# Kernel tuning notes

Measured on AMD Instinct MI355X. Metric: run time of the kernel, lower is better.

The kernel has to match this reference:

```python
import jax, jax.numpy as jnp
import numpy as np

B = 8192
D = 1024        # input_size
HID = 1024      # hidden_size
H = 8           # num_heads
HS = HID // H   # head_size = 128
P = int(HID * (4.0 / 3.0))  # 1365
K = 4           # causal conv kernel size


def _linear_params(key, fan_in, shape_w, shape_b):
    kw, kb = jax.random.split(key)
    s = 1.0 / np.sqrt(fan_in)
    w = jax.random.uniform(kw, shape_w, jnp.float32, -s, s)
    b = jax.random.uniform(kb, shape_b, jnp.float32, -s, s)
    return w, b


def setup_inputs() -> dict:
    key = jax.random.key(0)
    ks = jax.random.split(key, 20)
    inp = {
        'x': jax.random.normal(ks[0], (B, D), jnp.float32),
        'h_prev': jax.random.normal(ks[1], (B, HID), jnp.float32),
        'c_prev': jnp.zeros((B, HID), jnp.float32),
        'n_prev': jnp.ones((B, HID), jnp.float32),
        'm_prev': jnp.zeros((B, HID), jnp.float32),
        'rms_w': jnp.ones((D,), jnp.float32),
    }
    # causal conv: Conv1d(1,1,4) -> weight [4], bias scalar
    cw, cb = _linear_params(ks[2], K, (K,), ())
    inp['conv_w'], inp['conv_b'] = cw, cb
    # block-diagonal input projections: [H, D/H, HID/H] stored as x @ W (already transposed)
    names_in = ['Wz', 'Wi', 'Wf', 'Wo']
    for i, nm in enumerate(names_in):
        w, b = _linear_params(ks[3 + i], D // H, (H, D // H, HS), (HID,))
        inp[nm + '_w'], inp[nm + '_b'] = w, b
    names_rec = ['Rz', 'Ri', 'Rf', 'Ro']
    for i, nm in enumerate(names_rec):
        w, b = _linear_params(ks[7 + i], HS, (H, HS, HS), (HID,))
        inp[nm + '_w'], inp[nm + '_b'] = w, b
    inp['gn_w'] = jnp.ones((HID,), jnp.float32)
    inp['gn_b'] = jnp.zeros((HID,), jnp.float32)
    w, b = _linear_params(ks[11], HID, (HID, P), (P,))
    inp['upL_w'], inp['upL_b'] = w, b
    w, b = _linear_params(ks[12], HID, (HID, P), (P,))
    inp['upR_w'], inp['upR_b'] = w, b
    w, b = _linear_params(ks[13], P, (P, D), (D,))
    inp['down_w'], inp['down_b'] = w, b
    return inp


def _block_diag(x, w, b, num_blocks):
    # x: [B, F_in]; w: [H, F_in/H, F_out/H]; b: [F_out]
    bsz = x.shape[0]
    xh = x.reshape(bsz, num_blocks, -1)
    y = jnp.einsum('bhd,hde->bhe', xh, w)
    return y.reshape(bsz, -1) + b


def _rmsnorm(x, w, eps=1e-6):
    return x * jax.lax.rsqrt(jnp.mean(x * x, axis=-1, keepdims=True) + eps) * w


def _groupnorm(x, w, b, num_groups, eps=1e-5):
    bsz, C = x.shape
    xg = x.reshape(bsz, num_groups, -1)
    mu = jnp.mean(xg, axis=-1, keepdims=True)
    var = jnp.mean(jnp.square(xg - mu), axis=-1, keepdims=True)
    xn = (xg - mu) * jax.lax.rsqrt(var + eps)
    return xn.reshape(bsz, C) * w + b


def _causal_conv(x, w, b):
    # x: [B, L]; cross-correlation with left pad K-1 (matches Conv1d pad=3 then [:-3])
    L = x.shape[1]
    xp = jnp.pad(x, ((0, 0), (K - 1, 0)))
    out = b
    for k in range(K):
        out = out + w[k] * xp[:, k:k + L]
    return out


def reference(x, h_prev, c_prev, n_prev, m_prev, rms_w, conv_w, conv_b,
              Wz_w, Wz_b, Wi_w, Wi_b, Wf_w, Wf_b, Wo_w, Wo_b,
              Rz_w, Rz_b, Ri_w, Ri_b, Rf_w, Rf_b, Ro_w, Ro_b,
              gn_w, gn_b, upL_w, upL_b, upR_w, upR_b, down_w, down_b):
    x_norm = _rmsnorm(x, rms_w)
    x_conv = jax.nn.silu(_causal_conv(x_norm, conv_w, conv_b))

    z = jnp.tanh(_block_diag(x, Wz_w, Wz_b, H) + _block_diag(h_prev, Rz_w, Rz_b, H))
    o = jax.nn.sigmoid(_block_diag(x, Wo_w, Wo_b, H) + _block_diag(h_prev, Ro_w, Ro_b, H))
    i_tilde = _block_diag(x_conv, Wi_w, Wi_b, H) + _block_diag(h_prev, Ri_w, Ri_b, H)
    f_tilde = _block_diag(x_conv, Wf_w, Wf_b, H) + _block_diag(h_prev, Rf_w, Rf_b, H)

    m_t = jnp.maximum(f_tilde + m_prev, i_tilde)
    i_g = jnp.exp(i_tilde - m_t)
    f_g = jnp.exp(f_tilde + m_prev - m_t)
    c_t = f_g * c_prev + i_g * z
    n_t = f_g * n_prev + i_g
    h_t = o * c_t / n_t

    out_norm = _groupnorm(h_t, gn_w, gn_b, H)
    left = out_norm @ upL_w + upL_b
    right = out_norm @ upR_w + upR_b
    out = (left * jax.nn.gelu(right, approximate=False)) @ down_w + down_b
    final_output = out + x
    return (final_output, h_t, c_t, n_t, m_t)
```

## Files before the change

### kernel.cpp

```cpp
#include <hip/hip_runtime.h>
#include <hip/hip_bf16.h>
#include <math.h>

typedef __attribute__((ext_vector_type(8))) short bf16x8;
typedef __attribute__((ext_vector_type(4))) float f32x4;

#define BSZ   8192
#define DIM   1024
#define HIDN  1024
#define NH    8
#define HSZ   128
#define PN    1365
#define PPAD  1408

#define MFMA16(a, b, c) __builtin_amdgcn_mfma_f32_16x16x32_bf16(a, b, c, 0, 0, 0)

__device__ __forceinline__ void gload_lds16(const void* g, void* l) {
    __builtin_amdgcn_global_load_lds(
        (const __attribute__((address_space(1))) unsigned int*)(unsigned long long)g,
        (__attribute__((address_space(3))) unsigned int*)(unsigned int)(unsigned long long)l,
        16, 0, 0);
}

__device__ __forceinline__ void split_bf16(float v, __hip_bfloat16* hi, __hip_bfloat16* lo) {
    __hip_bfloat16 h = __float2bfloat16(v);
    *hi = h;
    *lo = __float2bfloat16(v - __bfloat162float(h));
}

__global__ __launch_bounds__(256) void k_rms_conv(
    const float* __restrict__ x, const float* __restrict__ rms_w,
    const float* __restrict__ conv_w, const float* __restrict__ conv_b,
    float* __restrict__ x_conv)
{
    __shared__ float xn[3 + DIM];
    __shared__ float red[4];
    const int row = blockIdx.x;
    const int t = threadIdx.x;
    const float* xr = x + (size_t)row * DIM;

    float4 v = *(const float4*)(xr + t * 4);
    float ss = v.x * v.x + v.y * v.y + v.z * v.z + v.w * v.w;
    #pragma unroll
    for (int off = 32; off; off >>= 1) ss += __shfl_down(ss, off);
    if ((t & 63) == 0) red[t >> 6] = ss;
    if (t < 3) xn[t] = 0.0f;
    __syncthreads();
    float tot = red[0] + red[1] + red[2] + red[3];
    float scale = rsqrtf(tot * (1.0f / (float)DIM) + 1e-6f);

    float4 w = *(const float4*)(rms_w + t * 4);
    xn[3 + t * 4 + 0] = v.x * scale * w.x;
    xn[3 + t * 4 + 1] = v.y * scale * w.y;
    xn[3 + t * 4 + 2] = v.z * scale * w.z;
    xn[3 + t * 4 + 3] = v.w * scale * w.w;
    __syncthreads();

    const float cw0 = conv_w[0], cw1 = conv_w[1], cw2 = conv_w[2], cw3 = conv_w[3];
    const float cb = conv_b[0];
    float4 o;
    float* op = (float*)&o;
    #pragma unroll
    for (int j = 0; j < 4; ++j) {
        int l = t * 4 + j;
        float val = cb + cw0 * xn[l] + cw1 * xn[l + 1] + cw2 * xn[l + 2] + cw3 * xn[l + 3];
        op[j] = val * (1.0f / (1.0f + expf(-val)));
    }
    *(float4*)(x_conv + (size_t)row * DIM + t * 4) = o;
}

#define TB2 16
__global__ __launch_bounds__(256) void k_gates(
    const float* __restrict__ x, const float* __restrict__ h_prev,
    const float* __restrict__ c_prev, const float* __restrict__ n_prev,
    const float* __restrict__ m_prev, const float* __restrict__ xconv,
    const float* __restrict__ Wz, const float* __restrict__ Wzb,
    const float* __restrict__ Wi, const float* __restrict__ Wib,
    const float* __restrict__ Wf, const float* __restrict__ Wfb,
    const float* __restrict__ Wo, const float* __restrict__ Wob,
    const float* __restrict__ Rz, const float* __restrict__ Rzb,
    const float* __restrict__ Ri, const float* __restrict__ Rib,
    const float* __restrict__ Rf, const float* __restrict__ Rfb,
    const float* __restrict__ Ro, const float* __restrict__ Rob,
    const float* __restrict__ gn_w, const float* __restrict__ gn_b,
    float* __restrict__ out_h, float* __restrict__ out_c,
    float* __restrict__ out_n, float* __restrict__ out_m,
    __hip_bfloat16* __restrict__ on_hi, __hip_bfloat16* __restrict__ on_lo)
{
    __shared__ float xs[TB2][HSZ];
    __shared__ float xc[TB2][HSZ];
    __shared__ float hs[TB2][HSZ];
    __shared__ float musig[TB2][2];

    const int h = blockIdx.y;
    const int rb = blockIdx.x * TB2;
    const int t = threadIdx.x;

    for (int i = t; i < TB2 * 32; i += 256) {
        int r = i >> 5, c4 = (i & 31) * 4;
        size_t g = (size_t)(rb + r) * DIM + h * HSZ + c4;
        *(float4*)&xs[r][c4] = *(const float4*)(x + g);
        *(float4*)&xc[r][c4] = *(const float4*)(xconv + g);
        *(float4*)&hs[r][c4] = *(const float4*)(h_prev + g);
    }
    __syncthreads();

    const int e = t & 127;
    const int r2 = t >> 7;
    const int hb = h * (HSZ * HSZ) + e;
    const float *pWz = Wz + hb, *pWi = Wi + hb, *pWf = Wf + hb, *pWo = Wo + hb;
    const float *pRz = Rz + hb, *pRi = Ri + hb, *pRf = Rf + hb, *pRo = Ro + hb;

    float az[8] = {}, ai_[8] = {}, af_[8] = {}, ao_[8] = {};

    for (int d0 = 0; d0 < HSZ; d0 += 4) {
        float wz[4], wi[4], wf[4], wo[4], rz[4], ri[4], rf[4], ro[4];
        #pragma unroll
        for (int j = 0; j < 4; ++j) {
            int off = (d0 + j) * HSZ;
            wz[j] = pWz[off]; wi[j] = pWi[off]; wf[j] = pWf[off]; wo[j] = pWo[off];
            rz[j] = pRz[off]; ri[j] = pRi[off]; rf[j] = pRf[off]; ro[j] = pRo[off];
        }
        #pragma unroll
        for (int k2 = 0; k2 < 8; ++k2) {
            int r = (r2 << 3) + k2;
            float4 xv = *(const float4*)&xs[r][d0];
            float4 cv = *(const float4*)&xc[r][d0];
            float4 hv = *(const float4*)&hs[r][d0];
            float xa[4] = {xv.x, xv.y, xv.z, xv.w};
            float ca[4] = {cv.x, cv.y, cv.z, cv.w};
            float ha[4] = {hv.x, hv.y, hv.z, hv.w};
            #pragma unroll
            for (int j = 0; j < 4; ++j) {
                az[k2]  = fmaf(xa[j], wz[j], fmaf(ha[j], rz[j], az[k2]));
                ao_[k2] = fmaf(xa[j], wo[j], fmaf(ha[j], ro[j], ao_[k2]));
                ai_[k2] = fmaf(ca[j], wi[j], fmaf(ha[j], ri[j], ai_[k2]));
                af_[k2] = fmaf(ca[j], wf[j], fmaf(ha[j], rf[j], af_[k2]));
            }
        }
    }

    const int col = h * HSZ + e;
    const float bz = Wzb[col] + Rzb[col];
    const float bi = Wib[col] + Rib[col];
    const float bf = Wfb[col] + Rfb[col];
    const float bo = Wob[col] + Rob[col];

    __syncthreads();

    #pragma unroll
    for (int k2 = 0; k2 < 8; ++k2) {
        int r = (r2 << 3) + k2;
        size_t gi = (size_t)(rb + r) * HIDN + col;
        float cp = c_prev[gi], np = n_prev[gi], mp = m_prev[gi];
        float zg = tanhf(az[k2] + bz);
        float og = 1.0f / (1.0f + expf(-(ao_[k2] + bo)));
        float it = ai_[k2] + bi;
        float ft = af_[k2] + bf;
        float mt = fmaxf(ft + mp, it);
        float ig = expf(it - mt);
        float fg = expf(ft + mp - mt);
        float ct = fg * cp + ig * zg;
        float nt = fg * np + ig;
        float ht = og * ct / nt;
        out_m[gi] = mt; out_c[gi] = ct; out_n[gi] = nt; out_h[gi] = ht;
        xs[r][e] = ht;
    }
    __syncthreads();

    {
        const int s = t & 15, row = t >> 4;
        float sum = 0.0f, sq = 0.0f;
        #pragma unroll
        for (int j = 0; j < 8; ++j) {
            float v = xs[row][s + 16 * j];
            sum += v; sq += v * v;
        }
        #pragma unroll
        for (int off = 8; off; off >>= 1) {
            sum += __shfl_xor(sum, off);
            sq  += __shfl_xor(sq, off);
        }
        if (s == 0) {
            float mu = sum * (1.0f / 128.0f);
            float var = sq * (1.0f / 128.0f) - mu * mu;
            musig[row][0] = mu;
            musig[row][1] = rsqrtf(var + 1e-5f);
        }
    }
    __syncthreads();

    const float gw = gn_w[col], gb = gn_b[col];
    #pragma unroll
    for (int k2 = 0; k2 < 8; ++k2) {
        int r = (r2 << 3) + k2;
        float on = (xs[r][e] - musig[r][0]) * musig[r][1] * gw + gb;
        size_t o = (size_t)(rb + r) * HIDN + col;
        __hip_bfloat16 hi, lo;
        split_bf16(on, &hi, &lo);
        on_hi[o] = hi; on_lo[o] = lo;
    }
}

__global__ __launch_bounds__(256) void k_tconv(
    const float* __restrict__ src, int K, int N, int Kpad, int Npad,
    __hip_bfloat16* __restrict__ dhi, __hip_bfloat16* __restrict__ dlo)
{
    __shared__ float tile[32][33];
    const int bk = blockIdx.x * 32;
    const int bn = blockIdx.y * 32;
    const int t = threadIdx.x;
    #pragma unroll
    for (int i = 0; i < 4; ++i) {
        int idx = t + i * 256; int r = idx >> 5, c = idx & 31;
        int gk = bk + r, gn = bn + c;
        float v = 0.0f;
        if (gk < K && gn < N) v = src[(size_t)gk * N + gn];
        tile[r][c] = v;
    }
    __syncthreads();
    #pragma unroll
    for (int i = 0; i < 4; ++i) {
        int idx = t + i * 256; int r = idx >> 5, c = idx & 31;
        int gn = bn + r, gk = bk + c;
        if (gn < Npad && gk < Kpad) {
            float v = tile[c][r];
            __hip_bfloat16 hi, lo;
            split_bf16(v, &hi, &lo);
            size_t o = (size_t)gn * Kpad + gk;
            dhi[o] = hi; dlo[o] = lo;
        }
    }
}

#define U_AHI 0
#define U_ALO 8192
#define U_BLH 16384
#define U_BLL 20480
#define U_BRH 24576
#define U_BRL 28672
__global__ __launch_bounds__(256, 2) void k_up(
    const __hip_bfloat16* __restrict__ on_hi, const __hip_bfloat16* __restrict__ on_lo,
    const __hip_bfloat16* __restrict__ wLhi, const __hip_bfloat16* __restrict__ wLlo,
    const __hip_bfloat16* __restrict__ wRhi, const __hip_bfloat16* __restrict__ wRlo,
    const float* __restrict__ bL, const float* __restrict__ bR,
    __hip_bfloat16* __restrict__ ff_hi, __hip_bfloat16* __restrict__ ff_lo)
{
    __shared__ __align__(16) char smem[32768];
    const int t = threadIdx.x;
    const int bm = blockIdx.x * 128;
    const int bn = blockIdx.y * 64;

    const int srow = t >> 2, sslot = (t & 3) * 8;
    const __hip_bfloat16* pAh = on_hi + (size_t)(bm + srow) * 1024 + sslot;
    const __hip_bfloat16* pAl = on_lo + (size_t)(bm + srow) * 1024 + sslot;
    const __hip_bfloat16* pLh = wLhi + (size_t)(bn + srow) * 1024 + sslot;
    const __hip_bfloat16* pLl = wLlo + (size_t)(bn + srow) * 1024 + sslot;
    const __hip_bfloat16* pRh = wRhi + (size_t)(bn + srow) * 1024 + sslot;
    const __hip_bfloat16* pRl = wRlo + (size_t)(bn + srow) * 1024 + sslot;

    const int lane = t & 63, l15 = lane & 15, l4 = lane >> 4;
    const int wave = t >> 6;
    const int wm = (wave >> 1) * 64, wn = (wave & 1) * 32;
    const int aoff = (wm + l15) * 64 + l4 * 16;
    const int boff = (wn + l15) * 64 + l4 * 16;

    f32x4 accL[4][2] = {};
    f32x4 accR[4][2] = {};

    for (int k0 = 0; k0 < 1024; k0 += 32) {
        gload_lds16(pAh + k0,          smem + U_AHI + t * 16);
        gload_lds16(pAh + 65536 + k0,  smem + U_AHI + 4096 + t * 16);
        gload_lds16(pAl + k0,          smem + U_ALO + t * 16);
        gload_lds16(pAl + 65536 + k0,  smem + U_ALO + 4096 + t * 16);
        gload_lds16(pLh + k0,          smem + U_BLH + t * 16);
        gload_lds16(pLl + k0,          smem + U_BLL + t * 16);
        gload_lds16(pRh + k0,          smem + U_BRH + t * 16);
        gload_lds16(pRl + k0,          smem + U_BRL + t * 16);
        __syncthreads();

        bf16x8 ah[4], al[4];
        #pragma unroll
        for (int mr = 0; mr < 4; ++mr) {
            ah[mr] = *(const bf16x8*)(smem + U_AHI + aoff + mr * 1024);
            al[mr] = *(const bf16x8*)(smem + U_ALO + aoff + mr * 1024);
        }
        #pragma unroll
        for (int nr = 0; nr < 2; ++nr) {
            bf16x8 blh = *(const bf16x8*)(smem + U_BLH + boff + nr * 1024);
            bf16x8 bll = *(const bf16x8*)(smem + U_BLL + boff + nr * 1024);
            bf16x8 brh = *(const bf16x8*)(smem + U_BRH + boff + nr * 1024);
            bf16x8 brl = *(const bf16x8*)(smem + U_BRL + boff + nr * 1024);
            #pragma unroll
            for (int mr = 0; mr < 4; ++mr) {
                accL[mr][nr] = MFMA16(ah[mr], blh, accL[mr][nr]);
                accL[mr][nr] = MFMA16(al[mr], blh, accL[mr][nr]);
                accL[mr][nr] = MFMA16(ah[mr], bll, accL[mr][nr]);
                accR[mr][nr] = MFMA16(ah[mr], brh, accR[mr][nr]);
                accR[mr][nr] = MFMA16(al[mr], brh, accR[mr][nr]);
                accR[mr][nr] = MFMA16(ah[mr], brl, accR[mr][nr]);
            }
        }
        __syncthreads();
    }

    #pragma unroll
    for (int mr = 0; mr < 4; ++mr) {
        #pragma unroll
        for (int nr = 0; nr < 2; ++nr) {
            int n = bn + wn + nr * 16 + l15;
            bool valid = n < PN;
            float bLv = valid ? bL[n] : 0.0f;
            float bRv = valid ? bR[n] : 0.0f;
            #pragma unroll
            for (int j = 0; j < 4; ++j) {
                int row = bm + wm + mr * 16 + l4 * 4 + j;
                size_t o = (size_t)row * PPAD + n;
                float v = 0.0f;
                if (valid) {
                    float lf = accL[mr][nr][j] + bLv;
                    float rf = accR[mr][nr][j] + bRv;
                    float g = 0.5f * rf * (1.0f + erff(rf * 0.70710678f));
                    v = lf * g;
                }
                __hip_bfloat16 hi, lo;
                split_bf16(v, &hi, &lo);
                ff_hi[o] = hi; ff_lo[o] = lo;
            }
        }
    }
}

#define D_AHI 0
#define D_ALO 8192
#define D_BHI 16384
#define D_BLO 24576
__global__ __launch_bounds__(256, 2) void k_down(
    const __hip_bfloat16* __restrict__ ff_hi, const __hip_bfloat16* __restrict__ ff_lo,
    const __hip_bfloat16* __restrict__ dwhi, const __hip_bfloat16* __restrict__ dwlo,
    const float* __restrict__ db, const float* __restrict__ x,
    float* __restrict__ out)
{
    __shared__ __align__(16) char smem[32768];
    const int t = threadIdx.x;
    const int bm = blockIdx.x * 128;
    const int bn = blockIdx.y * 128;

    const int srow = t >> 2, sslot = (t & 3) * 8;
    const __hip_bfloat16* pAh = ff_hi + (size_t)(bm + srow) * PPAD + sslot;
    const __hip_bfloat16* pAl = ff_lo + (size_t)(bm + srow) * PPAD + sslot;
    const __hip_bfloat16* pBh = dwhi + (size_t)(bn + srow) * PPAD + sslot;
    const __hip_bfloat16* pBl = dwlo + (size_t)(bn + srow) * PPAD + sslot;
    const int rstep = 64 * PPAD;

    const int lane = t & 63, l15 = lane & 15, l4 = lane >> 4;
    const int wave = t >> 6;
    const int wm = (wave >> 1) * 64, wn = (wave & 1) * 64;
    const int aoff = (wm + l15) * 64 + l4 * 16;
    const int boff = (wn + l15) * 64 + l4 * 16;

    f32x4 acc[4][4] = {};

    for (int k0 = 0; k0 < PPAD; k0 += 32) {
        gload_lds16(pAh + k0,         smem + D_AHI + t * 16);
        gload_lds16(pAh + rstep + k0, smem + D_AHI + 4096 + t * 16);
        gload_lds16(pAl + k0,         smem + D_ALO + t * 16);
        gload_lds16(pAl + rstep + k0, smem + D_ALO + 4096 + t * 16);
        gload_lds16(pBh + k0,         smem + D_BHI + t * 16);
        gload_lds16(pBh + rstep + k0, smem + D_BHI + 4096 + t * 16);
        gload_lds16(pBl + k0,         smem + D_BLO + t * 16);
        gload_lds16(pBl + rstep + k0, smem + D_BLO + 4096 + t * 16);
        __syncthreads();

        bf16x8 ah[4], al[4];
        #pragma unroll
        for (int mr = 0; mr < 4; ++mr) {
            ah[mr] = *(const bf16x8*)(smem + D_AHI + aoff + mr * 1024);
            al[mr] = *(const bf16x8*)(smem + D_ALO + aoff + mr * 1024);
        }
        #pragma unroll
        for (int nr = 0; nr < 4; ++nr) {
            bf16x8 bh = *(const bf16x8*)(smem + D_BHI + boff + nr * 1024);
            bf16x8 bl = *(const bf16x8*)(smem + D_BLO + boff + nr * 1024);
            #pragma unroll
            for (int mr = 0; mr < 4; ++mr) {
                acc[mr][nr] = MFMA16(ah[mr], bh, acc[mr][nr]);
                acc[mr][nr] = MFMA16(al[mr], bh, acc[mr][nr]);
                acc[mr][nr] = MFMA16(ah[mr], bl, acc[mr][nr]);
            }
        }
        __syncthreads();
    }

    #pragma unroll
    for (int mr = 0; mr < 4; ++mr) {
        #pragma unroll
        for (int nr = 0; nr < 4; ++nr) {
            int col = bn + wn + nr * 16 + l15;
            float dbv = db[col];
            #pragma unroll
            for (int j = 0; j < 4; ++j) {
                int row = bm + wm + mr * 16 + l4 * 4 + j;
                size_t o = (size_t)row * HIDN + col;
                out[o] = acc[mr][nr][j] + dbv + x[o];
            }
        }
    }
}

extern "C" void kernel_launch(void* const* d_in, const int* in_sizes, int n_in,
                              void* d_out, int out_size, void* d_ws, size_t ws_size,
                              hipStream_t stream) {
    const float* x      = (const float*)d_in[0];
    const float* h_prev = (const float*)d_in[1];
    const float* c_prev = (const float*)d_in[2];
    const float* n_prev = (const float*)d_in[3];
    const float* m_prev = (const float*)d_in[4];
    const float* rms_w  = (const float*)d_in[5];
    const float* conv_w = (const float*)d_in[6];
    const float* conv_b = (const float*)d_in[7];
    const float* Wz_w = (const float*)d_in[8],  *Wz_b = (const float*)d_in[9];
    const float* Wi_w = (const float*)d_in[10], *Wi_b = (const float*)d_in[11];
    const float* Wf_w = (const float*)d_in[12], *Wf_b = (const float*)d_in[13];
    const float* Wo_w = (const float*)d_in[14], *Wo_b = (const float*)d_in[15];
    const float* Rz_w = (const float*)d_in[16], *Rz_b = (const float*)d_in[17];
    const float* Ri_w = (const float*)d_in[18], *Ri_b = (const float*)d_in[19];
    const float* Rf_w = (const float*)d_in[20], *Rf_b = (const float*)d_in[21];
    const float* Ro_w = (const float*)d_in[22], *Ro_b = (const float*)d_in[23];
    const float* gn_w = (const float*)d_in[24], *gn_b = (const float*)d_in[25];
    const float* upL_w = (const float*)d_in[26], *upL_b = (const float*)d_in[27];
    const float* upR_w = (const float*)d_in[28], *upR_b = (const float*)d_in[29];
    const float* down_w = (const float*)d_in[30], *down_b = (const float*)d_in[31];

    float* out_final = (float*)d_out;
    float* out_h = out_final + (size_t)BSZ * HIDN;
    float* out_c = out_h + (size_t)BSZ * HIDN;
    float* out_n = out_c + (size_t)BSZ * HIDN;
    float* out_m = out_n + (size_t)BSZ * HIDN;
    __hip_bfloat16* on_hi = (__hip_bfloat16*)out_final;
    __hip_bfloat16* on_lo = on_hi + (size_t)BSZ * HIDN;

    const size_t NEEDED_WS = 63438848ull;
    if (ws_size < NEEDED_WS) {
        return;
    }
    char* wsb = (char*)d_ws;
    float* x_conv = (float*)wsb;
    __hip_bfloat16* ff_hi = (__hip_bfloat16*)wsb;
    __hip_bfloat16* ff_lo = (__hip_bfloat16*)(wsb + 23068672ull);
    __hip_bfloat16* wLhi  = (__hip_bfloat16*)(wsb + 46137344ull);
    __hip_bfloat16* wLlo  = (__hip_bfloat16*)(wsb + 49020928ull);
    __hip_bfloat16* wRhi  = (__hip_bfloat16*)(wsb + 51904512ull);
    __hip_bfloat16* wRlo  = (__hip_bfloat16*)(wsb + 54788096ull);
    __hip_bfloat16* dwhi  = (__hip_bfloat16*)(wsb + 57671680ull);
    __hip_bfloat16* dwlo  = (__hip_bfloat16*)(wsb + 60555264ull);

    k_tconv<<<dim3(32, 44), 256, 0, stream>>>(upL_w, 1024, PN, 1024, PPAD, wLhi, wLlo);
    k_tconv<<<dim3(32, 44), 256, 0, stream>>>(upR_w, 1024, PN, 1024, PPAD, wRhi, wRlo);
    k_tconv<<<dim3(44, 32), 256, 0, stream>>>(down_w, PN, 1024, PPAD, 1024, dwhi, dwlo);

    k_rms_conv<<<dim3(BSZ), 256, 0, stream>>>(x, rms_w, conv_w, conv_b, x_conv);

    k_gates<<<dim3(BSZ / TB2, NH), 256, 0, stream>>>(
        x, h_prev, c_prev, n_prev, m_prev, x_conv,
        Wz_w, Wz_b, Wi_w, Wi_b, Wf_w, Wf_b, Wo_w, Wo_b,
        Rz_w, Rz_b, Ri_w, Ri_b, Rf_w, Rf_b, Ro_w, Ro_b,
        gn_w, gn_b, out_h, out_c, out_n, out_m, on_hi, on_lo);

    k_up<<<dim3(BSZ / 128, PPAD / 64), 256, 0, stream>>>(
        on_hi, on_lo, wLhi, wLlo, wRhi, wRlo, upL_b, upR_b, ff_hi, ff_lo);

    k_down<<<dim3(BSZ / 128, HIDN / 128), 256, 0, stream>>>(
        ff_hi, ff_lo, dwhi, dwlo, down_b, x, out_final);
}
```

Measured before the change: 810.3 us.

## Move block-diagonal gate projections to split-bf16 MFMA with prepacked weights

The gate kernel previously computed the eight block-diagonal projections with scalar FP32 FMAs. It now uses bf16 hi/lo split MFMA, with three MFMAs per product to keep near-FP32 accuracy. A new pack kernel converts the W/R weights into an MFMA-fragment layout, and the RMS/conv kernel now emits bf16 hi/lo copies of x, x_conv and h_prev. Each wave handles one gate, and results are exchanged through shared memory in two phases before the xLSTM update and groupnorm. This trades extra workspace traffic for the bf16 activation copies and a weight-pack pass against much higher matrix throughput.

New measurement: 735.5 us. -9.2%, faster.

```diff
diff --git a/kernel.cpp b/kernel.cpp
--- a/kernel.cpp
+++ b/kernel.cpp
@@ -27,19 +27,34 @@
     *hi = h;
     *lo = __float2bfloat16(v - __bfloat162float(h));
 }
+__device__ __forceinline__ unsigned short bf_hi(float v) {
+    union { __hip_bfloat16 b; unsigned short u; } c;
+    c.b = __float2bfloat16(v);
+    return c.u;
+}
+__device__ __forceinline__ unsigned short bf_lo(float v) {
+    __hip_bfloat16 h = __float2bfloat16(v);
+    union { __hip_bfloat16 b; unsigned short u; } c;
+    c.b = __float2bfloat16(v - __bfloat162float(h));
+    return c.u;
+}
 
 __global__ __launch_bounds__(256) void k_rms_conv(
-    const float* __restrict__ x, const float* __restrict__ rms_w,
+    const float* __restrict__ x, const float* __restrict__ h_prev,
+    const float* __restrict__ rms_w,
     const float* __restrict__ conv_w, const float* __restrict__ conv_b,
-    float* __restrict__ x_conv)
+    unsigned short* __restrict__ xh_hi, unsigned short* __restrict__ xh_lo,
+    unsigned short* __restrict__ xch_hi, unsigned short* __restrict__ xch_lo,
+    unsigned short* __restrict__ hh_hi, unsigned short* __restrict__ hh_lo)
 {
     __shared__ float xn[3 + DIM];
     __shared__ float red[4];
     const int row = blockIdx.x;
     const int t = threadIdx.x;
-    const float* xr = x + (size_t)row * DIM;
-
-    float4 v = *(const float4*)(xr + t * 4);
+    const size_t base = (size_t)row * DIM + t * 4;
+
+    float4 v = *(const float4*)(x + base);
+    float4 hv = *(const float4*)(h_prev + base);
     float ss = v.x * v.x + v.y * v.y + v.z * v.z + v.w * v.w;
     #pragma unroll
     for (int off = 32; off; off >>= 1) ss += __shfl_down(ss, off);
@@ -54,133 +69,199 @@
     xn[3 + t * 4 + 1] = v.y * scale * w.y;
     xn[3 + t * 4 + 2] = v.z * scale * w.z;
     xn[3 + t * 4 + 3] = v.w * scale * w.w;
+
+    ushort4 ph, pl;
+    ph.x = bf_hi(v.x); ph.y = bf_hi(v.y); ph.z = bf_hi(v.z); ph.w = bf_hi(v.w);
+    pl.x = bf_lo(v.x); pl.y = bf_lo(v.y); pl.z = bf_lo(v.z); pl.w = bf_lo(v.w);
+    *(ushort4*)(xh_hi + base) = ph;
+    *(ushort4*)(xh_lo + base) = pl;
+    ph.x = bf_hi(hv.x); ph.y = bf_hi(hv.y); ph.z = bf_hi(hv.z); ph.w = bf_hi(hv.w);
+    pl.x = bf_lo(hv.x); pl.y = bf_lo(hv.y); pl.z = bf_lo(hv.z); pl.w = bf_lo(hv.w);
+    *(ushort4*)(hh_hi + base) = ph;
+    *(ushort4*)(hh_lo + base) = pl;
     __syncthreads();
 
     const float cw0 = conv_w[0], cw1 = conv_w[1], cw2 = conv_w[2], cw3 = conv_w[3];
     const float cb = conv_b[0];
-    float4 o;
-    float* op = (float*)&o;
+    float o[4];
     #pragma unroll
     for (int j = 0; j < 4; ++j) {
         int l = t * 4 + j;
         float val = cb + cw0 * xn[l] + cw1 * xn[l + 1] + cw2 * xn[l + 2] + cw3 * xn[l + 3];
-        op[j] = val * (1.0f / (1.0f + expf(-val)));
-    }
-    *(float4*)(x_conv + (size_t)row * DIM + t * 4) = o;
-}
-
-#define TB2 16
-__global__ __launch_bounds__(256) void k_gates(
-    const float* __restrict__ x, const float* __restrict__ h_prev,
+        o[j] = val * (1.0f / (1.0f + expf(-val)));
+    }
+    ph.x = bf_hi(o[0]); ph.y = bf_hi(o[1]); ph.z = bf_hi(o[2]); ph.w = bf_hi(o[3]);
+    pl.x = bf_lo(o[0]); pl.y = bf_lo(o[1]); pl.z = bf_lo(o[2]); pl.w = bf_lo(o[3]);
+    *(ushort4*)(xch_hi + base) = ph;
+    *(ushort4*)(xch_lo + base) = pl;
+}
+
+__global__ __launch_bounds__(256) void k_gw_pack(
+    const float* __restrict__ Wz, const float* __restrict__ Wo,
+    const float* __restrict__ Wi, const float* __restrict__ Wf,
+    const float* __restrict__ Rz, const float* __restrict__ Ro,
+    const float* __restrict__ Ri, const float* __restrict__ Rf,
+    unsigned short* __restrict__ wgp_hi, unsigned short* __restrict__ wgp_lo)
+{
+    __shared__ float tile[32][129];
+    const int ks = blockIdx.x;
+    const int hg = blockIdx.y;
+    const int h = hg >> 2, g = hg & 3;
+    const float* W = (g == 0) ? Wz : (g == 1) ? Wo : (g == 2) ? Wi : Wf;
+    const float* R = (g == 0) ? Rz : (g == 1) ? Ro : (g == 2) ? Ri : Rf;
+    const float* src = ((ks < 4) ? W : R) + h * 16384 + ((ks & 3) * 32) * 128;
+    const int t = threadIdx.x;
+    #pragma unroll
+    for (int i = 0; i < 16; ++i) {
+        int idx = t + i * 256;
+        tile[idx >> 7][idx & 127] = src[(idx >> 7) * 128 + (idx & 127)];
+    }
+    __syncthreads();
+    const size_t obase = ((size_t)hg * 8 + ks) * 4096;
+    #pragma unroll
+    for (int i = 0; i < 16; ++i) {
+        int oidx = t + i * 256;
+        int ni = oidx >> 9, lane = (oidx >> 3) & 63, j = oidx & 7;
+        int nl = lane & 15, kl = (lane >> 4) * 8 + j;
+        float v = tile[kl][ni * 16 + nl];
+        wgp_hi[obase + oidx] = bf_hi(v);
+        wgp_lo[obase + oidx] = bf_lo(v);
+    }
+}
+
+__global__ __launch_bounds__(256, 2) void k_gates(
+    const unsigned short* __restrict__ xh_hi, const unsigned short* __restrict__ xh_lo,
+    const unsigned short* __restrict__ xch_hi, const unsigned short* __restrict__ xch_lo,
+    const unsigned short* __restrict__ hh_hi, const unsigned short* __restrict__ hh_lo,
+    const unsigned short* __restrict__ wgp_hi, const unsigned short* __restrict__ wgp_lo,
+    const float* __restrict__ Wzb, const float* __restrict__ Wob,
+    const float* __restrict__ Wib, const float* __restrict__ Wfb,
+    const float* __restrict__ Rzb, const float* __restrict__ Rob,
+    const float* __restrict__ Rib, const float* __restrict__ Rfb,
     const float* __restrict__ c_prev, const float* __restrict__ n_prev,
-    const float* __restrict__ m_prev, const float* __restrict__ xconv,
-    const float* __restrict__ Wz, const float* __restrict__ Wzb,
-    const float* __restrict__ Wi, const float* __restrict__ Wib,
-    const float* __restrict__ Wf, const float* __restrict__ Wfb,
-    const float* __restrict__ Wo, const float* __restrict__ Wob,
-    const float* __restrict__ Rz, const float* __restrict__ Rzb,
-    const float* __restrict__ Ri, const float* __restrict__ Rib,
-    const float* __restrict__ Rf, const float* __restrict__ Rfb,
-    const float* __restrict__ Ro, const float* __restrict__ Rob,
+    const float* __restrict__ m_prev,
     const float* __restrict__ gn_w, const float* __restrict__ gn_b,
     float* __restrict__ out_h, float* __restrict__ out_c,
     float* __restrict__ out_n, float* __restrict__ out_m,
     __hip_bfloat16* __restrict__ on_hi, __hip_bfloat16* __restrict__ on_lo)
 {
-    __shared__ float xs[TB2][HSZ];
-    __shared__ float xc[TB2][HSZ];
-    __shared__ float hs[TB2][HSZ];
-    __shared__ float musig[TB2][2];
-
+    __shared__ float GL[2][32][132];
+    __shared__ float musig[32][2];
+
+    const int t = threadIdx.x;
     const int h = blockIdx.y;
-    const int rb = blockIdx.x * TB2;
-    const int t = threadIdx.x;
-
-    for (int i = t; i < TB2 * 32; i += 256) {
-        int r = i >> 5, c4 = (i & 31) * 4;
-        size_t g = (size_t)(rb + r) * DIM + h * HSZ + c4;
-        *(float4*)&xs[r][c4] = *(const float4*)(x + g);
-        *(float4*)&xc[r][c4] = *(const float4*)(xconv + g);
-        *(float4*)&hs[r][c4] = *(const float4*)(h_prev + g);
+    const int rb = blockIdx.x * 32;
+    const int g = t >> 6;
+    const int lane = t & 63, l15 = lane & 15, l4 = lane >> 4;
+    const int hg = h * 4 + g;
+
+    const unsigned short* a1h = (g < 2) ? xh_hi : xch_hi;
+    const unsigned short* a1l = (g < 2) ? xh_lo : xch_lo;
+
+    f32x4 acc[2][8] = {};
+    const size_t rowA0 = (size_t)(rb + l15) * 1024 + h * 128 + l4 * 8;
+    const size_t rowA1 = rowA0 + (size_t)16 * 1024;
+
+#define GSTEP(SH, SL, KS)                                                      \
+    {                                                                          \
+        const int kk = ((KS) & 3) * 32;                                        \
+        bf16x8 f0h = *(const bf16x8*)((SH) + rowA0 + kk);                      \
+        bf16x8 f0l = *(const bf16x8*)((SL) + rowA0 + kk);                      \
+        bf16x8 f1h = *(const bf16x8*)((SH) + rowA1 + kk);                      \
+        bf16x8 f1l = *(const bf16x8*)((SL) + rowA1 + kk);                      \
+        _Pragma("unroll")                                                      \
+        for (int ni = 0; ni < 8; ++ni) {                                       \
+            size_t bo = (((size_t)hg * 8 + (KS)) * 8 + ni) * 512 + lane * 8;   \
+            bf16x8 bh = *(const bf16x8*)(wgp_hi + bo);                         \
+            bf16x8 bl = *(const bf16x8*)(wgp_lo + bo);                         \
+            acc[0][ni] = MFMA16(f0h, bh, acc[0][ni]);                          \
+            acc[0][ni] = MFMA16(f0l, bh, acc[0][ni]);                          \
+            acc[0][ni] = MFMA16(f0h, bl, acc[0][ni]);                          \
+            acc[1][ni] = MFMA16(f1h, bh, acc[1][ni]);                          \
+            acc[1][ni] = MFMA16(f1l, bh, acc[1][ni]);                          \
+            acc[1][ni] = MFMA16(f1h, bl, acc[1][ni]);                          \
+        }                                                                      \
+    }
+
+    GSTEP(a1h, a1l, 0) GSTEP(a1h, a1l, 1) GSTEP(a1h, a1l, 2) GSTEP(a1h, a1l, 3)
+    GSTEP(hh_hi, hh_lo, 4) GSTEP(hh_hi, hh_lo, 5)
+    GSTEP(hh_hi, hh_lo, 6) GSTEP(hh_hi, hh_lo, 7)
+#undef GSTEP
+
+    if (g < 2) {
+        #pragma unroll
+        for (int mi = 0; mi < 2; ++mi)
+            #pragma unroll
+            for (int ni = 0; ni < 8; ++ni)
+                #pragma unroll
+                for (int r = 0; r < 4; ++r)
+                    GL[g][mi * 16 + l4 * 4 + r][ni * 16 + l15] = acc[mi][ni][r];
     }
     __syncthreads();
 
     const int e = t & 127;
     const int r2 = t >> 7;
-    const int hb = h * (HSZ * HSZ) + e;
-    const float *pWz = Wz + hb, *pWi = Wi + hb, *pWf = Wf + hb, *pWo = Wo + hb;
-    const float *pRz = Rz + hb, *pRi = Ri + hb, *pRf = Rf + hb, *pRo = Ro + hb;
-
-    float az[8] = {}, ai_[8] = {}, af_[8] = {}, ao_[8] = {};
-
-    for (int d0 = 0; d0 < HSZ; d0 += 4) {
-        float wz[4], wi[4], wf[4], wo[4], rz[4], ri[4], rf[4], ro[4];
-        #pragma unroll
-        for (int j = 0; j < 4; ++j) {
-            int off = (d0 + j) * HSZ;
-            wz[j] = pWz[off]; wi[j] = pWi[off]; wf[j] = pWf[off]; wo[j] = pWo[off];
-            rz[j] = pRz[off]; ri[j] = pRi[off]; rf[j] = pRf[off]; ro[j] = pRo[off];
-        }
-        #pragma unroll
-        for (int k2 = 0; k2 < 8; ++k2) {
-            int r = (r2 << 3) + k2;
-            float4 xv = *(const float4*)&xs[r][d0];
-            float4 cv = *(const float4*)&xc[r][d0];
-            float4 hv = *(const float4*)&hs[r][d0];
-            float xa[4] = {xv.x, xv.y, xv.z, xv.w};
-            float ca[4] = {cv.x, cv.y, cv.z, cv.w};
-            float ha[4] = {hv.x, hv.y, hv.z, hv.w};
+    const int col = h * 128 + e;
+    const float bz = Wzb[col] + Rzb[col];
+    const float bo_ = Wob[col] + Rob[col];
+    const float bi = Wib[col] + Rib[col];
+    const float bf_ = Wfb[col] + Rfb[col];
+
+    float zg[16], og[16];
+    #pragma unroll
+    for (int k2 = 0; k2 < 16; ++k2) {
+        int r = r2 * 16 + k2;
+        zg[k2] = tanhf(GL[0][r][e] + bz);
+        og[k2] = 1.0f / (1.0f + expf(-(GL[1][r][e] + bo_)));
+    }
+    __syncthreads();
+
+    if (g >= 2) {
+        #pragma unroll
+        for (int mi = 0; mi < 2; ++mi)
             #pragma unroll
-            for (int j = 0; j < 4; ++j) {
-                az[k2]  = fmaf(xa[j], wz[j], fmaf(ha[j], rz[j], az[k2]));
-                ao_[k2] = fmaf(xa[j], wo[j], fmaf(ha[j], ro[j], ao_[k2]));
-                ai_[k2] = fmaf(ca[j], wi[j], fmaf(ha[j], ri[j], ai_[k2]));
-                af_[k2] = fmaf(ca[j], wf[j], fmaf(ha[j], rf[j], af_[k2]));
-            }
-        }
-    }
-
-    const int col = h * HSZ + e;
-    const float bz = Wzb[col] + Rzb[col];
-    const float bi = Wib[col] + Rib[col];
-    const float bf = Wfb[col] + Rfb[col];
-    const float bo = Wob[col] + Rob[col];
-
-    __syncthreads();
-
-    #pragma unroll
-    for (int k2 = 0; k2 < 8; ++k2) {
-        int r = (r2 << 3) + k2;
+            for (int ni = 0; ni < 8; ++ni)
+                #pragma unroll
+                for (int r = 0; r < 4; ++r)
+                    GL[g - 2][mi * 16 + l4 * 4 + r][ni * 16 + l15] = acc[mi][ni][r];
+    }
+    __syncthreads();
+
+    float htv[16];
+    #pragma unroll
+    for (int k2 = 0; k2 < 16; ++k2) {
+        int r = r2 * 16 + k2;
         size_t gi = (size_t)(rb + r) * HIDN + col;
+        float it = GL[0][r][e] + bi;
+        float ft = GL[1][r][e] + bf_;
         float cp = c_prev[gi], np = n_prev[gi], mp = m_prev[gi];
-        float zg = tanhf(az[k2] + bz);
-        float og = 1.0f / (1.0f + expf(-(ao_[k2] + bo)));
-        float it = ai_[k2] + bi;
-        float ft = af_[k2] + bf;
         float mt = fmaxf(ft + mp, it);
         float ig = expf(it - mt);
         float fg = expf(ft + mp - mt);
-        float ct = fg * cp + ig * zg;
+        float ct = fg * cp + ig * zg[k2];
         float nt = fg * np + ig;
-        float ht = og * ct / nt;
+        float ht = og[k2] * ct / nt;
         out_m[gi] = mt; out_c[gi] = ct; out_n[gi] = nt; out_h[gi] = ht;
-        xs[r][e] = ht;
-    }
+        htv[k2] = ht;
+    }
+    __syncthreads();
+
+    #pragma unroll
+    for (int k2 = 0; k2 < 16; ++k2)
+        GL[0][r2 * 16 + k2][e] = htv[k2];
     __syncthreads();
 
     {
-        const int s = t & 15, row = t >> 4;
+        const int s = t & 7, row = t >> 3;
         float sum = 0.0f, sq = 0.0f;
         #pragma unroll
-        for (int j = 0; j < 8; ++j) {
-            float v = xs[row][s + 16 * j];
+        for (int j = 0; j < 16; ++j) {
+            float v = GL[0][row][s + 8 * j];
             sum += v; sq += v * v;
         }
-        #pragma unroll
-        for (int off = 8; off; off >>= 1) {
-            sum += __shfl_xor(sum, off);
-            sq  += __shfl_xor(sq, off);
-        }
+        sum += __shfl_xor(sum, 4); sq += __shfl_xor(sq, 4);
+        sum += __shfl_xor(sum, 2); sq += __shfl_xor(sq, 2);
+        sum += __shfl_xor(sum, 1); sq += __shfl_xor(sq, 1);
         if (s == 0) {
             float mu = sum * (1.0f / 128.0f);
             float var = sq * (1.0f / 128.0f) - mu * mu;
@@ -192,9 +273,9 @@
 
     const float gw = gn_w[col], gb = gn_b[col];
     #pragma unroll
-    for (int k2 = 0; k2 < 8; ++k2) {
-        int r = (r2 << 3) + k2;
-        float on = (xs[r][e] - musig[r][0]) * musig[r][1] * gw + gb;
+    for (int k2 = 0; k2 < 16; ++k2) {
+        int r = r2 * 16 + k2;
+        float on = (GL[0][r][e] - musig[r][0]) * musig[r][1] * gw + gb;
         size_t o = (size_t)(rb + r) * HIDN + col;
         __hip_bfloat16 hi, lo;
         split_bf16(on, &hi, &lo);
@@ -320,8 +401,8 @@
                 if (valid) {
                     float lf = accL[mr][nr][j] + bLv;
                     float rf = accR[mr][nr][j] + bRv;
-                    float g = 0.5f * rf * (1.0f + erff(rf * 0.70710678f));
-                    v = lf * g;
+                    float gg = 0.5f * rf * (1.0f + erff(rf * 0.70710678f));
+                    v = lf * gg;
                 }
                 __hip_bfloat16 hi, lo;
                 split_bf16(v, &hi, &lo);
@@ -396,17 +477,35 @@
     for (int mr = 0; mr < 4; ++mr) {
         #pragma unroll
         for (int nr = 0; nr < 4; ++nr) {
-            int col = bn + wn + nr * 16 + l15;
-            float dbv = db[col];
+            int colc = bn + wn + nr * 16 + l15;
+            float dbv = db[colc];
             #pragma unroll
             for (int j = 0; j < 4; ++j) {
                 int row = bm + wm + mr * 16 + l4 * 4 + j;
-                size_t o = (size_t)row * HIDN + col;
+                size_t o = (size_t)row * HIDN + colc;
                 out[o] = acc[mr][nr][j] + dbv + x[o];
             }
         }
     }
 }
+
+#define WS_XH_HI   0ull
+#define WS_XH_LO   16777216ull
+#define WS_XCH_HI  33554432ull
+#define WS_XCH_LO  50331648ull
+#define WS_HH_HI   67108864ull
+#define WS_HH_LO   83886080ull
+#define WS_WGP_HI  100663296ull
+#define WS_WGP_LO  102760448ull
+#define WS_WL_HI   104857600ull
+#define WS_WL_LO   107741184ull
+#define WS_WR_HI   110624768ull
+#define WS_WR_LO   113508352ull
+#define WS_DW_HI   116391936ull
+#define WS_DW_LO   119275520ull
+#define WS_END     122159104ull
+#define WS_FF_HI   0ull
+#define WS_FF_LO   23068672ull
 
 extern "C" void kernel_launch(void* const* d_in, const int* in_sizes, int n_in,
                               void* d_out, int out_size, void* d_ws, size_t ws_size,
@@ -440,32 +539,42 @@
     __hip_bfloat16* on_hi = (__hip_bfloat16*)out_final;
     __hip_bfloat16* on_lo = on_hi + (size_t)BSZ * HIDN;
 
-    const size_t NEEDED_WS = 63438848ull;
-    if (ws_size < NEEDED_WS) {
-        return;
-    }
+    if (ws_size < WS_END) return;
+
     char* wsb = (char*)d_ws;
-    float* x_conv = (float*)wsb;
-    __hip_bfloat16* ff_hi = (__hip_bfloat16*)wsb;
-    __hip_bfloat16* ff_lo = (__hip_bfloat16*)(wsb + 23068672ull);
-    __hip_bfloat16* wLhi  = (__hip_bfloat16*)(wsb + 46137344ull);
-    __hip_bfloat16* wLlo  = (__hip_bfloat16*)(wsb + 49020928ull);
-    __hip_bfloat16* wRhi  = (__hip_bfloat16*)(wsb + 51904512ull);
-    __hip_bfloat16* wRlo  = (__hip_bfloat16*)(wsb + 54788096ull);
-    __hip_bfloat16* dwhi  = (__hip_bfloat16*)(wsb + 57671680ull);
-    __hip_bfloat16* dwlo  = (__hip_bfloat16*)(wsb + 60555264ull);
+    unsigned short* xh_hi  = (unsigned short*)(wsb + WS_XH_HI);
+    unsigned short* xh_lo  = (unsigned short*)(wsb + WS_XH_LO);
+    unsigned short* xch_hi = (unsigned short*)(wsb + WS_XCH_HI);
+    unsigned short* xch_lo = (unsigned short*)(wsb + WS_XCH_LO);
+    unsigned short* hh_hi  = (unsigned short*)(wsb + WS_HH_HI);
+    unsigned short* hh_lo  = (unsigned short*)(wsb + WS_HH_LO);
+    unsigned short* wgp_hi = (unsigned short*)(wsb + WS_WGP_HI);
+    unsigned short* wgp_lo = (unsigned short*)(wsb + WS_WGP_LO);
+    __hip_bfloat16* wLhi   = (__hip_bfloat16*)(wsb + WS_WL_HI);
+    __hip_bfloat16* wLlo   = (__hip_bfloat16*)(wsb + WS_WL_LO);
+    __hip_bfloat16* wRhi   = (__hip_bfloat16*)(wsb + WS_WR_HI);
+    __hip_bfloat16* wRlo   = (__hip_bfloat16*)(wsb + WS_WR_LO);
+    __hip_bfloat16* dwhi   = (__hip_bfloat16*)(wsb + WS_DW_HI);
+    __hip_bfloat16* dwlo   = (__hip_bfloat16*)(wsb + WS_DW_LO);
+    __hip_bfloat16* ff_hi  = (__hip_bfloat16*)(wsb + WS_FF_HI);
+    __hip_bfloat16* ff_lo  = (__hip_bfloat16*)(wsb + WS_FF_LO);
+
+    k_gw_pack<<<dim3(8, 32), 256, 0, stream>>>(
+        Wz_w, Wo_w, Wi_w, Wf_w, Rz_w, Ro_w, Ri_w, Rf_w, wgp_hi, wgp_lo);
 
     k_tconv<<<dim3(32, 44), 256, 0, stream>>>(upL_w, 1024, PN, 1024, PPAD, wLhi, wLlo);
     k_tconv<<<dim3(32, 44), 256, 0, stream>>>(upR_w, 1024, PN, 1024, PPAD, wRhi, wRlo);
     k_tconv<<<dim3(44, 32), 256, 0, stream>>>(down_w, PN, 1024, PPAD, 1024, dwhi, dwlo);
 
-    k_rms_conv<<<dim3(BSZ), 256, 0, stream>>>(x, rms_w, conv_w, conv_b, x_conv);
-
-    k_gates<<<dim3(BSZ / TB2, NH), 256, 0, stream>>>(
-        x, h_prev, c_prev, n_prev, m_prev, x_conv,
-        Wz_w, Wz_b, Wi_w, Wi_b, Wf_w, Wf_b, Wo_w, Wo_b,
-        Rz_w, Rz_b, Ri_w, Ri_b, Rf_w, Rf_b, Ro_w, Ro_b,
-        gn_w, gn_b, out_h, out_c, out_n, out_m, on_hi, on_lo);
+    k_rms_conv<<<dim3(BSZ), 256, 0, stream>>>(
+        x, h_prev, rms_w, conv_w, conv_b,
+        xh_hi, xh_lo, xch_hi, xch_lo, hh_hi, hh_lo);
+
+    k_gates<<<dim3(BSZ / 32, NH), 256, 0, stream>>>(
+        xh_hi, xh_lo, xch_hi, xch_lo, hh_hi, hh_lo, wgp_hi, wgp_lo,
+        Wz_b, Wo_b, Wi_b, Wf_b, Rz_b, Ro_b, Ri_b, Rf_b,
+        c_prev, n_prev, m_prev, gn_w, gn_b,
+        out_h, out_c, out_n, out_m, on_hi, on_lo);
 
     k_up<<<dim3(BSZ / 128, PPAD / 64), 256, 0, stream>>>(
         on_hi, on_lo, wLhi, wLlo, wRhi, wRlo, upL_b, upR_b, ff_hi, ff_lo);
```
